# Performance work log

Hardware: AMD Instinct MI355X
Metric: run time of the kernel (lower is better)

The kernel has to match this reference:

```python
import jax, jax.numpy as jnp
import numpy as np

V = 10000   # vocab_size
L = 12      # n_layer
H = 12      # n_head
C = 768     # n_embd
TE = 64     # t_embd
WTE = C - TE
BS = 1024   # block_size
B, T = 4, 1024
D = C // H
EPS = 1e-5


def setup_inputs() -> dict:
    key = jax.random.key(0)
    ks = jax.random.split(key, 12)
    s = 0.02
    def n(k, shape, extra=1.0):
        return jax.random.normal(k, shape, jnp.float32) * (s * extra)
    resid_scale = 1.0 / np.sqrt(2 * L)  # c_proj init std scaling from _init_weights loop
    return {
        'idx': jax.random.randint(ks[0], (B, T), 0, V),
        'ts': jax.random.uniform(ks[1], (B, T), jnp.float32) * 100.0,
        'wte': n(ks[2], (V, WTE)),
        'basis_freq': jnp.asarray(1.0 / 10 ** np.linspace(0, 9, TE), jnp.float32),
        'phase': jnp.zeros((TE,), jnp.float32),
        'wpe': n(ks[3], (BS, C)),
        'ln1_w': jnp.ones((L, C), jnp.float32), 'ln1_b': jnp.zeros((L, C), jnp.float32),
        'qkv_w': n(ks[4], (L, 3 * C, C)), 'qkv_b': jnp.zeros((L, 3 * C), jnp.float32),
        'proj_w': n(ks[5], (L, C, C), resid_scale), 'proj_b': jnp.zeros((L, C), jnp.float32),
        'ln2_w': jnp.ones((L, C), jnp.float32), 'ln2_b': jnp.zeros((L, C), jnp.float32),
        'fc_w': n(ks[6], (L, 4 * C, C)), 'fc_b': jnp.zeros((L, 4 * C), jnp.float32),
        'fc2_w': n(ks[7], (L, C, 4 * C), resid_scale), 'fc2_b': jnp.zeros((L, C), jnp.float32),
        'lnf_w': jnp.ones((C,), jnp.float32), 'lnf_b': jnp.zeros((C,), jnp.float32),
        'lm_w': n(ks[8], (V, C)),
        'tp_w': n(ks[9], (1, C)),
    }


def _ln(x, w, b):
    mu = jnp.mean(x, -1, keepdims=True)
    var = jnp.mean((x - mu) ** 2, -1, keepdims=True)
    return (x - mu) * jax.lax.rsqrt(var + EPS) * w + b


def reference(idx, ts, wte, basis_freq, phase, wpe, ln1_w, ln1_b, qkv_w, qkv_b,
              proj_w, proj_b, ln2_w, ln2_b, fc_w, fc_b, fc2_w, fc2_b,
              lnf_w, lnf_b, lm_w, tp_w):
    Bv, Tv = idx.shape
    tok = wte[idx]                                      # [B,T,C-TE]
    tim = jnp.cos(ts[..., None] * basis_freq + phase)   # TimeEncode -> [B,T,TE]
    x = jnp.concatenate([tok, tim], axis=-1) + wpe[:Tv]
    mask = jnp.tril(jnp.ones((Tv, Tv), bool))
    scale = 1.0 / np.sqrt(D)

    def block(x, p):
        l1w, l1b, qw, qb, pw, pb, l2w, l2b, fw, fb, f2w, f2b = p
        h = _ln(x, l1w, l1b)
        qkv = h @ qw.T + qb                              # [B,T,3C]
        q, k, v = jnp.split(qkv, 3, axis=-1)
        def heads(z):
            return z.reshape(Bv, Tv, H, D).transpose(0, 2, 1, 3)  # [B,H,T,D]
        q, k, v = heads(q), heads(k), heads(v)
        att = jnp.einsum('bhtd,bhsd->bhts', q, k) * scale
        att = jnp.where(mask, att, -jnp.inf)             # causal masked_fill
        att = jax.nn.softmax(att, axis=-1)
        y = jnp.einsum('bhts,bhsd->bhtd', att, v)
        y = y.transpose(0, 2, 1, 3).reshape(Bv, Tv, C)
        x = x + (y @ pw.T + pb)
        h2 = _ln(x, l2w, l2b)
        m = jax.nn.gelu(h2 @ fw.T + fb, approximate=False)  # torch nn.GELU default is exact
        x = x + (m @ f2w.T + f2b)
        return x, None

    x, _ = jax.lax.scan(block, x, (ln1_w, ln1_b, qkv_w, qkv_b, proj_w, proj_b,
                                   ln2_w, ln2_b, fc_w, fc_b, fc2_w, fc2_b))
    x = _ln(x, lnf_w, lnf_b)
    logits = x @ lm_w.T          # [B,T,V]
    tpred = x @ tp_w.T           # [B,T,1]
    return logits, tpred
```

## Files before the change

kernel.cpp:

```cpp
#include <hip/hip_runtime.h>
#include <hip/hip_bf16.h>
#include <math.h>

#define Bb   4
#define Tt   1024
#define Cc   768
#define Hh   12
#define Dd   64
#define Ll   12
#define Vv   10000
#define WTEe 704
#define MTOT 4096

#define QSCALE 0.18033688f

typedef __bf16 bf16x8 __attribute__((ext_vector_type(8)));
typedef float  f32x4  __attribute__((ext_vector_type(4)));
typedef unsigned short u16;

typedef const __attribute__((address_space(1))) void* gptr_t;
typedef __attribute__((address_space(3))) void* lptr_t;

__device__ inline void gload16(const void* g, void* l) {
    __builtin_amdgcn_global_load_lds((gptr_t)g, (lptr_t)l, 16, 0, 0);
}

__device__ inline u16 f2bf(float f) {
    unsigned int u = __float_as_uint(f);
    return (u16)((u + 0x7fffu + ((u >> 16) & 1u)) >> 16);
}
__device__ inline float bf2f(u16 u) { return __uint_as_float(((unsigned)u) << 16); }

__device__ inline float gelu_f(float v) {
    float t = v * (0.797884561f + 0.0356774081f * v * v);
    float e = __expf(2.f * t);
    float th = 1.f - 2.f / (e + 1.f);
    return 0.5f * v * (1.f + th);
}

#if __has_builtin(__builtin_amdgcn_exp2f)
__device__ inline float fast_exp2(float x) { return __builtin_amdgcn_exp2f(x); }
#else
__device__ inline float fast_exp2(float x) { return exp2f(x); }
#endif

#define WAITVM(N)  asm volatile("s_waitcnt vmcnt(" #N ")" ::: "memory")
#define WAITLGKM0() asm volatile("s_waitcnt lgkmcnt(0)" ::: "memory")
#define SCHEDB()   __builtin_amdgcn_sched_barrier(0)
#define SBAR()     __builtin_amdgcn_s_barrier()

__global__ __launch_bounds__(256)
void convert_pack(const float* __restrict__ in, u16* __restrict__ out,
                  int nk8, int K, int rowmod, int scaleLim)
{
    int i = blockIdx.x * 256 + threadIdx.x;
    if (i >= nk8) return;
    int row = (i << 3) / K;
    int col = (i << 3) % K;
    float s = 1.f;
    if (rowmod && (row % rowmod) < scaleLim) s = QSCALE;
    float4 v0 = ((const float4*)in)[2 * i];
    float4 v1 = ((const float4*)in)[2 * i + 1];
    uint4 o;
    o.x = (unsigned)f2bf(v0.x * s) | ((unsigned)f2bf(v0.y * s) << 16);
    o.y = (unsigned)f2bf(v0.z * s) | ((unsigned)f2bf(v0.w * s) << 16);
    o.z = (unsigned)f2bf(v1.x * s) | ((unsigned)f2bf(v1.y * s) << 16);
    o.w = (unsigned)f2bf(v1.z * s) | ((unsigned)f2bf(v1.w * s) << 16);
    int tile = row >> 4, kt = col >> 5;
    int l = (row & 15) | (((col >> 3) & 3) << 4);
    size_t off = (((size_t)tile * (K >> 5) + kt) << 9) + l * 8;
    *(uint4*)(out + off) = o;
}

__global__ __launch_bounds__(256)
void scale_qkvb(const float* __restrict__ in, float* __restrict__ out, int n)
{
    int i = blockIdx.x * 256 + threadIdx.x;
    if (i >= n) return;
    int col = i % (3 * Cc);
    out[i] = in[i] * (col < Cc ? QSCALE : 1.f);
}

__global__ __launch_bounds__(256)
void embed_kernel(const int* __restrict__ idx, const float* __restrict__ ts,
                  const float* __restrict__ wte, const float* __restrict__ freq,
                  const float* __restrict__ ph, const float* __restrict__ wpe,
                  float* __restrict__ x)
{
    const int bt  = blockIdx.x;
    const int t   = bt & (Tt - 1);
    const int tok = idx[bt];
    const float tv = ts[bt];
#pragma unroll
    for (int j = 0; j < 3; ++j) {
        int c = threadIdx.x + (j << 8);
        float val;
        if (c < WTEe) val = wte[(size_t)tok * WTEe + c];
        else {
            int e = c - WTEe;
            val = cosf(tv * freq[e] + ph[e]);
        }
        x[(size_t)bt * Cc + c] = val + wpe[(size_t)t * Cc + c];
    }
}

__global__ __launch_bounds__(256)
void ln_kernel(const float* __restrict__ x, const float* __restrict__ wt,
               const float* __restrict__ bs, u16* __restrict__ out)
{
    const int row = blockIdx.x;
    const int tid = threadIdx.x;
    const float* xr = x + (size_t)row * Cc;
    float v0 = xr[tid], v1 = xr[tid + 256], v2 = xr[tid + 512];
    float s = v0 + v1 + v2;
#pragma unroll
    for (int m = 32; m; m >>= 1) s += __shfl_xor(s, m);
    __shared__ float red[4];
    const int wv = tid >> 6;
    if ((tid & 63) == 0) red[wv] = s;
    __syncthreads();
    float mu = (red[0] + red[1] + red[2] + red[3]) * (1.f / 768.f);
    float d0 = v0 - mu, d1 = v1 - mu, d2 = v2 - mu;
    float s2 = d0 * d0 + d1 * d1 + d2 * d2;
#pragma unroll
    for (int m = 32; m; m >>= 1) s2 += __shfl_xor(s2, m);
    __syncthreads();
    if ((tid & 63) == 0) red[wv] = s2;
    __syncthreads();
    float var = (red[0] + red[1] + red[2] + red[3]) * (1.f / 768.f);
    float rs = rsqrtf(var + 1e-5f);
    u16* orow = out + (size_t)row * Cc;
    orow[tid]       = f2bf(d0 * rs * wt[tid]       + bs[tid]);
    orow[tid + 256] = f2bf(d1 * rs * wt[tid + 256] + bs[tid + 256]);
    orow[tid + 512] = f2bf(d2 * rs * wt[tid + 512] + bs[tid + 512]);
}

__device__ inline void st_out(float* p, size_t o, float v) { p[o] = v; }
__device__ inline void st_out(u16*   p, size_t o, float v) { p[o] = f2bf(v); }

template<int EPI, typename OutT>
__global__ __launch_bounds__(256)
void gemm_bf16(const u16* __restrict__ A, const u16* __restrict__ Wp,
               const float* __restrict__ bias, const float* __restrict__ resid,
               OutT* __restrict__ out, u16* __restrict__ vt, int N, int K)
{
    __shared__ uint4 AF[3][8][64];
    __shared__ uint4 BF[3][8][64];
    const int tid  = threadIdx.x;
    const int lane = tid & 63;
    const int w    = tid >> 6;
    const int wr   = w >> 1, wc = w & 1;
    const int lq   = lane & 15, g = lane >> 4;
    const int m0   = blockIdx.x * 128, n0 = blockIdx.y * 128;
    const int KB   = K >> 5;

    const int arow0 = m0 + (2 * w) * 16 + lq;
    const int arow1 = arow0 + 16;
    const u16* ap0 = A + (size_t)arow0 * K + g * 8;
    const u16* ap1 = A + (size_t)arow1 * K + g * 8;

    int tn0 = (n0 >> 4) + 2 * w, tn1 = tn0 + 1;
    const int tmax = (N >> 4) - 1;
    tn0 = tn0 < tmax ? tn0 : tmax;
    tn1 = tn1 < tmax ? tn1 : tmax;
    const u16* bq0 = Wp + (((size_t)tn0 * KB) << 9) + lane * 8;
    const u16* bq1 = Wp + (((size_t)tn1 * KB) << 9) + lane * 8;

    f32x4 acc[4][4] = {};
    const int nk = KB;

#define GSTAGE(s, sl) do { int kk_ = (s) << 5;                      \
        gload16(ap0 + kk_, &AF[sl][2 * w][lane]);                   \
        gload16(ap1 + kk_, &AF[sl][2 * w + 1][lane]);               \
        gload16(bq0 + ((size_t)(s) << 9), &BF[sl][2 * w][lane]);    \
        gload16(bq1 + ((size_t)(s) << 9), &BF[sl][2 * w + 1][lane]); } while (0)

    GSTAGE(0, 0);
    GSTAGE(1, 1);
    WAITVM(4);
    SCHEDB();
    SBAR();
    SCHEDB();

    int sl = 0;
    for (int t = 0; t < nk; ++t) {
        int sl2 = sl + 2; if (sl2 >= 3) sl2 -= 3;
        if (t + 2 < nk) GSTAGE(t + 2, sl2);

        bf16x8 af[4], bfr[4];
#pragma unroll
        for (int mi = 0; mi < 4; ++mi)
            af[mi] = __builtin_bit_cast(bf16x8, AF[sl][wr * 4 + mi][lane]);
#pragma unroll
        for (int ni = 0; ni < 4; ++ni)
            bfr[ni] = __builtin_bit_cast(bf16x8, BF[sl][wc * 4 + ni][lane]);
        __builtin_amdgcn_s_setprio(1);
#pragma unroll
        for (int mi = 0; mi < 4; ++mi)
#pragma unroll
            for (int ni = 0; ni < 4; ++ni)
                acc[mi][ni] = __builtin_amdgcn_mfma_f32_16x16x32_bf16(
                    af[mi], bfr[ni], acc[mi][ni], 0, 0, 0);
        __builtin_amdgcn_s_setprio(0);

        if (t + 2 < nk) { WAITVM(4); }
        else           { WAITVM(0); }
        SCHEDB();
        SBAR();
        SCHEDB();
        sl = (sl + 1 == 3) ? 0 : sl + 1;
    }
#undef GSTAGE

    if (EPI == 3 && n0 >= 1536) {
#pragma unroll
        for (int mi = 0; mi < 4; ++mi)
#pragma unroll
            for (int ni = 0; ni < 4; ++ni) {
                int col = n0 + wc * 64 + ni * 16 + lq;
                int c2  = col - 1536;
                int hh  = c2 >> 6, dd = c2 & 63;
                int row = m0 + wr * 64 + mi * 16 + g * 4;
                int bb  = row >> 10, tr = row & 1023;
                float bv = bias[col];
                ushort4 o;
                o.x = f2bf(acc[mi][ni][0] + bv);
                o.y = f2bf(acc[mi][ni][1] + bv);
                o.z = f2bf(acc[mi][ni][2] + bv);
                o.w = f2bf(acc[mi][ni][3] + bv);
                *(ushort4*)&vt[(((size_t)bb * Hh + hh) * Dd + dd) * Tt + tr] = o;
            }
        return;
    }

#pragma unroll
    for (int mi = 0; mi < 4; ++mi)
#pragma unroll
        for (int ni = 0; ni < 4; ++ni) {
            int col = n0 + wc * 64 + ni * 16 + lq;
            if (col >= N) continue;
            int row = m0 + wr * 64 + mi * 16 + g * 4;
            float bv = bias ? bias[col] : 0.f;
#pragma unroll
            for (int q = 0; q < 4; ++q) {
                float v = acc[mi][ni][q] + bv;
                size_t o = (size_t)(row + q) * N + col;
                if (EPI == 1) v += resid[o];
                if (EPI == 2) v = gelu_f(v);
                st_out(out, o, v);
            }
        }
}

template<int EPI, typename OutT>
__global__ __launch_bounds__(256)
void gemm_n64(const u16* __restrict__ A, const u16* __restrict__ Wp,
              const float* __restrict__ bias, const float* __restrict__ resid,
              OutT* __restrict__ out, int N, int K)
{
    __shared__ uint4 AF[3][4][64];
    __shared__ uint4 BF[3][8][64];
    const int tid  = threadIdx.x;
    const int lane = tid & 63;
    const int w    = tid >> 6;
    const int wr   = w & 1, wc = w >> 1;
    const int lq   = lane & 15, g = lane >> 4;
    const int m0   = blockIdx.x * 64, n0 = blockIdx.y * 128;
    const int KB   = K >> 5;

    const u16* ap  = A + (size_t)(m0 + w * 16 + lq) * K + g * 8;
    int tn0 = (n0 >> 4) + 2 * w, tn1 = tn0 + 1;
    const int tmax = (N >> 4) - 1;
    tn0 = tn0 < tmax ? tn0 : tmax;
    tn1 = tn1 < tmax ? tn1 : tmax;
    const u16* bq0 = Wp + (((size_t)tn0 * KB) << 9) + lane * 8;
    const u16* bq1 = Wp + (((size_t)tn1 * KB) << 9) + lane * 8;

    f32x4 acc[2][4] = {};
    const int nk = KB;

#define GSTAGE(s, sl) do { int kk_ = (s) << 5;                      \
        gload16(ap  + kk_, &AF[sl][w][lane]);                       \
        gload16(bq0 + ((size_t)(s) << 9), &BF[sl][2 * w][lane]);    \
        gload16(bq1 + ((size_t)(s) << 9), &BF[sl][2 * w + 1][lane]); } while (0)

    GSTAGE(0, 0);
    GSTAGE(1, 1);
    WAITVM(3);
    SCHEDB();
    SBAR();
    SCHEDB();

    int sl = 0;
    for (int t = 0; t < nk; ++t) {
        int sl2 = sl + 2; if (sl2 >= 3) sl2 -= 3;
        if (t + 2 < nk) GSTAGE(t + 2, sl2);

        bf16x8 af[2], bfr[4];
#pragma unroll
        for (int mi = 0; mi < 2; ++mi)
            af[mi] = __builtin_bit_cast(bf16x8, AF[sl][wr * 2 + mi][lane]);
#pragma unroll
        for (int ni = 0; ni < 4; ++ni)
            bfr[ni] = __builtin_bit_cast(bf16x8, BF[sl][wc * 4 + ni][lane]);
        __builtin_amdgcn_s_setprio(1);
#pragma unroll
        for (int mi = 0; mi < 2; ++mi)
#pragma unroll
            for (int ni = 0; ni < 4; ++ni)
                acc[mi][ni] = __builtin_amdgcn_mfma_f32_16x16x32_bf16(
                    af[mi], bfr[ni], acc[mi][ni], 0, 0, 0);
        __builtin_amdgcn_s_setprio(0);

        if (t + 2 < nk) { WAITVM(3); }
        else           { WAITVM(0); }
        SCHEDB();
        SBAR();
        SCHEDB();
        sl = (sl + 1 == 3) ? 0 : sl + 1;
    }
#undef GSTAGE

#pragma unroll
    for (int mi = 0; mi < 2; ++mi)
#pragma unroll
        for (int ni = 0; ni < 4; ++ni) {
            int col = n0 + wc * 64 + ni * 16 + lq;
            if (col >= N) continue;
            int row = m0 + wr * 32 + mi * 16 + g * 4;
            float bv = bias ? bias[col] : 0.f;
#pragma unroll
            for (int q = 0; q < 4; ++q) {
                float v = acc[mi][ni][q] + bv;
                size_t o = (size_t)(row + q) * N + col;
                if (EPI == 1) v += resid[o];
                if (EPI == 2) v = gelu_f(v);
                st_out(out, o, v);
            }
        }
}

template<int EPI, typename OutT>
__global__ __launch_bounds__(512, 2)
void gemm8p(const u16* __restrict__ A, const u16* __restrict__ Wp,
            const float* __restrict__ bias, const float* __restrict__ resid,
            OutT* __restrict__ out, int N, int K)
{
    __shared__ uint4 AF[2][16][2][64];
    __shared__ uint4 BF[2][16][2][64];
    const int tid  = threadIdx.x;
    const int lane = tid & 63;
    const int w    = tid >> 6;
    const int wr   = w >> 2, wc = w & 3;
    const int lq   = lane & 15, g = lane >> 4;
    const int m0   = blockIdx.x * 256, n0 = blockIdx.y * 256;
    const int KB   = K >> 5;

    const int ar0 = m0 + (2 * w) * 16 + lq;
    const u16* aS0 = A + (size_t)ar0 * K + g * 8;
    const u16* aS1 = aS0 + (size_t)16 * K;

    int tn0 = (n0 >> 4) + 2 * w, tn1 = tn0 + 1;
    const int tmax = (N >> 4) - 1;
    tn0 = tn0 < tmax ? tn0 : tmax;
    tn1 = tn1 < tmax ? tn1 : tmax;
    const u16* bq0 = Wp + (((size_t)tn0 * KB) << 9) + lane * 8;
    const u16* bq1 = Wp + (((size_t)tn1 * KB) << 9) + lane * 8;

    f32x4 acc[8][4] = {};
    const int nt = K >> 6;

    gload16(aS0,      &AF[0][2 * w][0][lane]);
    gload16(aS1,      &AF[0][2 * w + 1][0][lane]);
    gload16(bq0,                 &BF[0][2 * w][0][lane]);
    gload16(bq1,                 &BF[0][2 * w + 1][0][lane]);
    gload16(aS0 + 32, &AF[0][2 * w][1][lane]);
    gload16(aS1 + 32, &AF[0][2 * w + 1][1][lane]);
    gload16(bq0 + 512,           &BF[0][2 * w][1][lane]);
    gload16(bq1 + 512,           &BF[0][2 * w + 1][1][lane]);
    WAITVM(0);
    SCHEDB();
    SBAR();

    int buf = 0;
    for (int t = 0; t < nt; ++t) {
        const bool more = (t + 1 < nt);
        const int kn = (t + 1) << 6;
        const size_t bb0 = (size_t)(2 * (t + 1)) << 9;
        bf16x8 a0[4], a1[4], b0[4];

#pragma unroll
        for (int i = 0; i < 4; ++i)
            a0[i] = __builtin_bit_cast(bf16x8, AF[buf][wr * 8 + i][0][lane]);
#pragma unroll
        for (int i = 0; i < 4; ++i)
            b0[i] = __builtin_bit_cast(bf16x8, BF[buf][wc * 4 + i][0][lane]);
        if (more) {
            gload16(aS0 + kn, &AF[buf ^ 1][2 * w][0][lane]);
            gload16(aS1 + kn, &AF[buf ^ 1][2 * w + 1][0][lane]);
        }
        SCHEDB();
        SBAR();
        WAITLGKM0();
        SCHEDB();
        __builtin_amdgcn_s_setprio(1);
#pragma unroll
        for (int mi = 0; mi < 4; ++mi)
#pragma unroll
            for (int ni = 0; ni < 4; ++ni)
                acc[mi][ni] = __builtin_amdgcn_mfma_f32_16x16x32_bf16(
                    a0[mi], b0[ni], acc[mi][ni], 0, 0, 0);
        __builtin_amdgcn_s_setprio(0);
        SBAR();

#pragma unroll
        for (int i = 0; i < 4; ++i)
            a1[i] = __builtin_bit_cast(bf16x8, AF[buf][wr * 8 + 4 + i][0][lane]);
        if (more) {
            gload16(bq0 + bb0, &BF[buf ^ 1][2 * w][0][lane]);
            gload16(bq1 + bb0, &BF[buf ^ 1][2 * w + 1][0][lane]);
        }
        SCHEDB();
        SBAR();
        WAITLGKM0();
        SCHEDB();
        __builtin_amdgcn_s_setprio(1);
#pragma unroll
        for (int mi = 0; mi < 4; ++mi)
#pragma unroll
            for (int ni = 0; ni < 4; ++ni)
                acc[4 + mi][ni] = __builtin_amdgcn_mfma_f32_16x16x32_bf16(
                    a1[mi], b0[ni], acc[4 + mi][ni], 0, 0, 0);
        __builtin_amdgcn_s_setprio(0);
        if (more) { WAITVM(4); } else { WAITVM(0); }
        SCHEDB();
        SBAR();

#pragma unroll
        for (int i = 0; i < 4; ++i)
            a0[i] = __builtin_bit_cast(bf16x8, AF[buf][wr * 8 + i][1][lane]);
#pragma unroll
        for (int i = 0; i < 4; ++i)
            b0[i] = __builtin_bit_cast(bf16x8, BF[buf][wc * 4 + i][1][lane]);
        if (more) {
            gload16(aS0 + kn + 32, &AF[buf ^ 1][2 * w][1][lane]);
            gload16(aS1 + kn + 32, &AF[buf ^ 1][2 * w + 1][1][lane]);
        }
        SCHEDB();
        SBAR();
        WAITLGKM0();
        SCHEDB();
        __builtin_amdgcn_s_setprio(1);
#pragma unroll
        for (int mi = 0; mi < 4; ++mi)
#pragma unroll
            for (int ni = 0; ni < 4; ++ni)
                acc[mi][ni] = __builtin_amdgcn_mfma_f32_16x16x32_bf16(
                    a0[mi], b0[ni], acc[mi][ni], 0, 0, 0);
        __builtin_amdgcn_s_setprio(0);
        SBAR();

#pragma unroll
        for (int i = 0; i < 4; ++i)
            a1[i] = __builtin_bit_cast(bf16x8, AF[buf][wr * 8 + 4 + i][1][lane]);
        if (more) {
            gload16(bq0 + bb0 + 512, &BF[buf ^ 1][2 * w][1][lane]);
            gload16(bq1 + bb0 + 512, &BF[buf ^ 1][2 * w + 1][1][lane]);
        }
        SCHEDB();
        SBAR();
        WAITLGKM0();
        SCHEDB();
        __builtin_amdgcn_s_setprio(1);
#pragma unroll
        for (int mi = 0; mi < 4; ++mi)
#pragma unroll
            for (int ni = 0; ni < 4; ++ni)
                acc[4 + mi][ni] = __builtin_amdgcn_mfma_f32_16x16x32_bf16(
                    a1[mi], b0[ni], acc[4 + mi][ni], 0, 0, 0);
        __builtin_amdgcn_s_setprio(0);
        if (more) { WAITVM(4); } else { WAITVM(0); }
        SCHEDB();
        SBAR();

        buf ^= 1;
    }

#pragma unroll
    for (int mi = 0; mi < 8; ++mi)
#pragma unroll
        for (int ni = 0; ni < 4; ++ni) {
            int col = n0 + wc * 64 + ni * 16 + lq;
            if (col >= N) continue;
            int row = m0 + wr * 128 + mi * 16 + g * 4;
            float bv = bias ? bias[col] : 0.f;
#pragma unroll
            for (int q = 0; q < 4; ++q) {
                float v = acc[mi][ni][q] + bv;
                size_t o = (size_t)(row + q) * N + col;
                if (EPI == 1) v += resid[o];
                if (EPI == 2) v = gelu_f(v);
                st_out(out, o, v);
            }
        }
}

__global__ __launch_bounds__(512)
void attn_mfma(const u16* __restrict__ qkv, const u16* __restrict__ vt,
               u16* __restrict__ y)
{
    __shared__ uint4 KF[2][4][2][64];
    __shared__ uint4 VF[2][4][2][64];

    const int tid  = threadIdx.x;
    const int lane = tid & 63;
    const int w    = tid >> 6;
    const int lq   = lane & 15, g = lane >> 4;
    const int m    = gridDim.x - 1 - blockIdx.x;
    const int bh   = blockIdx.y;
    const int b    = bh / Hh, h = bh % Hh;
    const int wq0  = m * 128 + w * 16;
    const size_t base = (size_t)b * Tt * (3 * Cc);

    const u16* qrow = qkv + base + (size_t)(wq0 + lq) * (3 * Cc) + h * Dd;
    bf16x8 qf0 = __builtin_bit_cast(bf16x8, *(const uint4*)(qrow + g * 8));
    bf16x8 qf1 = __builtin_bit_cast(bf16x8, *(const uint4*)(qrow + 32 + g * 8));

    f32x4 yac[4] = {};
    float lrun = 0.f;

    const int wm = w & 3;
    const u16* kbase = qkv + base + Cc + h * Dd + (size_t)(wm * 16 + lq) * (3 * Cc) + g * 8;
    const u16* vbase = vt + ((size_t)bh * Dd + wm * 16 + lq) * Tt + g * 8;

#define STAGE(c, bi)  do {                                              \
        if (w < 4) {                                                    \
            const u16* kp = kbase + (size_t)(c) * 64 * (3 * Cc);        \
            gload16(kp,      &KF[bi][wm][0][lane]);                     \
            gload16(kp + 32, &KF[bi][wm][1][lane]);                     \
        } else {                                                        \
            const u16* vp = vbase + (c) * 64;                           \
            gload16(vp,      &VF[bi][wm][0][lane]);                     \
            gload16(vp + 32, &VF[bi][wm][1][lane]);                     \
        }                                                               \
    } while (0)

    const int nch = 2 * m + 2;
    STAGE(0, 0);
    WAITVM(0);
    SCHEDB();
    SBAR();

    const int srcb = lq + ((g & 1) << 5);

    int buf = 0;
    for (int c = 0; c < nch; ++c) {
        if (c + 1 < nch) STAGE(c + 1, buf ^ 1);

        f32x4 sc[4] = {};
        __builtin_amdgcn_s_setprio(1);
#pragma unroll
        for (int nt = 0; nt < 4; ++nt) {
            bf16x8 k0 = __builtin_bit_cast(bf16x8, KF[buf][nt][0][lane]);
            bf16x8 k1 = __builtin_bit_cast(bf16x8, KF[buf][nt][1][lane]);
            sc[nt] = __builtin_amdgcn_mfma_f32_16x16x32_bf16(k0, qf0, sc[nt], 0, 0, 0);
            sc[nt] = __builtin_amdgcn_mfma_f32_16x16x32_bf16(k1, qf1, sc[nt], 0, 0, 0);
        }
        __builtin_amdgcn_s_setprio(0);

        const int s0 = c * 64;
        if (s0 + 63 > wq0) {
            const int qg = wq0 + lq;
#pragma unroll
            for (int nt = 0; nt < 4; ++nt) {
                const int kb = s0 + nt * 16 + (g << 2);
#pragma unroll
                for (int j = 0; j < 4; ++j)
                    if (kb + j > qg) sc[nt][j] = -1e30f;
            }
        }

        float ls = 0.f;
#pragma unroll
        for (int nt = 0; nt < 4; ++nt)
#pragma unroll
            for (int j = 0; j < 4; ++j) {
                float p = fast_exp2(sc[nt][j]);
                sc[nt][j] = p;
                ls += p;
            }
        ls += __shfl_xor(ls, 16);
        ls += __shfl_xor(ls, 32);
        lrun += ls;

        unsigned pk[4][2];
#pragma unroll
        for (int nt = 0; nt < 4; ++nt) {
            unsigned u0 = __float_as_uint(sc[nt][0]);
            unsigned u1 = __float_as_uint(sc[nt][1]);
            unsigned u2 = __float_as_uint(sc[nt][2]);
            unsigned u3 = __float_as_uint(sc[nt][3]);
            pk[nt][0] = (u0 >> 16) | (u1 & 0xffff0000u);
            pk[nt][1] = (u2 >> 16) | (u3 & 0xffff0000u);
        }

        unsigned pa0[4], pa1[4];
#pragma unroll
        for (int m2 = 0; m2 < 4; ++m2) {
            int hsel = m2 & 1;
            int src  = srcb + ((m2 >> 1) << 4);
            unsigned lo0 = __shfl(pk[0][hsel], src);
            unsigned hi0 = __shfl(pk[1][hsel], src);
            unsigned lo1 = __shfl(pk[2][hsel], src);
            unsigned hi1 = __shfl(pk[3][hsel], src);
            pa0[m2] = (g >> 1) ? hi0 : lo0;
            pa1[m2] = (g >> 1) ? hi1 : lo1;
        }
        uint4 A0 = make_uint4(pa0[0], pa0[1], pa0[2], pa0[3]);
        uint4 A1 = make_uint4(pa1[0], pa1[1], pa1[2], pa1[3]);
        bf16x8 pA0 = __builtin_bit_cast(bf16x8, A0);
        bf16x8 pA1 = __builtin_bit_cast(bf16x8, A1);

        __builtin_amdgcn_s_setprio(1);
#pragma unroll
        for (int dt = 0; dt < 4; ++dt) {
            bf16x8 vb0 = __builtin_bit_cast(bf16x8, VF[buf][dt][0][lane]);
            bf16x8 vb1 = __builtin_bit_cast(bf16x8, VF[buf][dt][1][lane]);
            yac[dt] = __builtin_amdgcn_mfma_f32_16x16x32_bf16(pA0, vb0, yac[dt], 0, 0, 0);
            yac[dt] = __builtin_amdgcn_mfma_f32_16x16x32_bf16(pA1, vb1, yac[dt], 0, 0, 0);
        }
        __builtin_amdgcn_s_setprio(0);

        if (c + 1 < nch) { WAITVM(0); }
        SCHEDB();
        SBAR();
        buf ^= 1;
    }
#undef STAGE

    f32x4 rl;
#pragma unroll
    for (int j = 0; j < 4; ++j)
        rl[j] = 1.0f / __shfl(lrun, (g << 2) + j);
#pragma unroll
    for (int dt = 0; dt < 4; ++dt)
#pragma unroll
        for (int j = 0; j < 4; ++j)
            y[(size_t)(b * Tt + wq0 + (g << 2) + j) * Cc + h * Dd + dt * 16 + lq]
                = f2bf(yac[dt][j] * rl[j]);
}

__global__ __launch_bounds__(256)
void tpred_kernel(const u16* __restrict__ h, const float* __restrict__ tp,
                  float* __restrict__ out)
{
    const int row  = blockIdx.x * 4 + (threadIdx.x >> 6);
    const int lane = threadIdx.x & 63;
    const u16* hr = h + (size_t)row * Cc;
    float s = 0.f;
#pragma unroll
    for (int j = 0; j < 12; ++j) s += bf2f(hr[lane + (j << 6)]) * tp[lane + (j << 6)];
#pragma unroll
    for (int m = 32; m; m >>= 1) s += __shfl_xor(s, m);
    if (lane == 0) out[row] = s;
}

extern "C" void kernel_launch(void* const* d_in, const int* in_sizes, int n_in,
                              void* d_out, int out_size, void* d_ws, size_t ws_size,
                              hipStream_t stream)
{
    const int*   idx  = (const int*)d_in[0];
    const float* ts   = (const float*)d_in[1];
    const float* wte  = (const float*)d_in[2];
    const float* freq = (const float*)d_in[3];
    const float* ph   = (const float*)d_in[4];
    const float* wpe  = (const float*)d_in[5];
    const float* ln1w = (const float*)d_in[6];
    const float* ln1b = (const float*)d_in[7];
    const float* qkvw = (const float*)d_in[8];
    const float* qkvb = (const float*)d_in[9];
    const float* pw   = (const float*)d_in[10];
    const float* pb   = (const float*)d_in[11];
    const float* ln2w = (const float*)d_in[12];
    const float* ln2b = (const float*)d_in[13];
    const float* fcw  = (const float*)d_in[14];
    const float* fcb  = (const float*)d_in[15];
    const float* f2w  = (const float*)d_in[16];
    const float* f2b  = (const float*)d_in[17];
    const float* lnfw = (const float*)d_in[18];
    const float* lnfb = (const float*)d_in[19];
    const float* lmw  = (const float*)d_in[20];
    const float* tpw  = (const float*)d_in[21];
    float* out = (float*)d_out;

    const int n_qkvw = 3 * Cc * Cc, n_pw = Cc * Cc, n_fcw = 4 * Cc * Cc;

    char* p = (char*)d_ws;
    float* x    = (float*)p;               p += (size_t)MTOT * Cc * 4;
    u16*   qkvB = (u16*)p;                 p += (size_t)MTOT * 3 * Cc * 2;
    u16*   VtB  = (u16*)p;                 p += (size_t)Bb * Hh * Dd * Tt * 2;
    u16*   hB   = (u16*)p;                 p += (size_t)MTOT * Cc * 2;
    u16*   yB   = (u16*)p;                 p += (size_t)MTOT * Cc * 2;
    u16*   mbB  = (u16*)p;                 p += (size_t)MTOT * 4 * Cc * 2;
    u16*   lmwB = (u16*)p;                 p += (size_t)Vv * Cc * 2;
    float* sbias= (float*)p;               p += (size_t)Ll * 3 * Cc * 4;
    char* wbase = p;

    size_t need_big = (size_t)(wbase - (char*)d_ws)
                    + ((size_t)Ll * (n_qkvw + n_pw + 2 * n_fcw)) * 2;
    bool big = ws_size >= need_big;

    u16 *wqA, *wpA, *wfA, *wf2A;
    if (big) {
        wqA  = (u16*)wbase;                wbase += (size_t)Ll * n_qkvw * 2;
        wpA  = (u16*)wbase;                wbase += (size_t)Ll * n_pw * 2;
        wfA  = (u16*)wbase;                wbase += (size_t)Ll * n_fcw * 2;
        wf2A = (u16*)wbase;
    } else {
        wqA  = (u16*)wbase;                wbase += (size_t)n_qkvw * 2;
        wpA  = (u16*)wbase;                wbase += (size_t)n_pw * 2;
        wfA  = (u16*)wbase;                wbase += (size_t)n_fcw * 2;
        wf2A = (u16*)wbase;
    }

    auto pack = [&](const float* src, u16* dst, size_t rows, int K,
                    int rowmod, int scaleLim) {
        int nk8 = (int)(rows * K / 8);
        convert_pack<<<(nk8 + 255) / 256, 256, 0, stream>>>(
            src, dst, nk8, K, rowmod, scaleLim);
    };

    pack(lmw, lmwB, Vv, Cc, 0, 0);
    {
        int nb = Ll * 3 * Cc;
        scale_qkvb<<<(nb + 255) / 256, 256, 0, stream>>>(qkvb, sbias, nb);
    }
    if (big) {
        pack(qkvw, wqA,  (size_t)Ll * 3 * Cc, Cc, 3 * Cc, Cc);
        pack(pw,   wpA,  (size_t)Ll * Cc,     Cc, 0, 0);
        pack(fcw,  wfA,  (size_t)Ll * 4 * Cc, Cc, 0, 0);
        pack(f2w,  wf2A, (size_t)Ll * Cc, 4 * Cc, 0, 0);
    }
    embed_kernel<<<MTOT, 256, 0, stream>>>(idx, ts, wte, freq, ph, wpe, x);

    for (int l = 0; l < Ll; ++l) {
        u16 *wqB, *wpB, *wfB, *wf2B;
        if (big) {
            wqB  = wqA  + (size_t)l * n_qkvw;
            wpB  = wpA  + (size_t)l * n_pw;
            wfB  = wfA  + (size_t)l * n_fcw;
            wf2B = wf2A + (size_t)l * n_fcw;
        } else {
            wqB = wqA; wpB = wpA; wfB = wfA; wf2B = wf2A;
            pack(qkvw + (size_t)l * n_qkvw, wqB, 3 * Cc, Cc, 3 * Cc, Cc);
            pack(pw   + (size_t)l * n_pw,   wpB, Cc,     Cc, 0, 0);
            pack(fcw  + (size_t)l * n_fcw,  wfB, 4 * Cc, Cc, 0, 0);
            pack(f2w  + (size_t)l * n_fcw,  wf2B, Cc, 4 * Cc, 0, 0);
        }

        ln_kernel<<<MTOT, 256, 0, stream>>>(x, ln1w + l * Cc, ln1b + l * Cc, hB);
        gemm_bf16<3, u16><<<dim3(32, 18), 256, 0, stream>>>(
            hB, wqB, sbias + (size_t)l * 3 * Cc, nullptr, qkvB, VtB, 3 * Cc, Cc);
        attn_mfma<<<dim3(Tt / 128, Bb * Hh), 512, 0, stream>>>(qkvB, VtB, yB);
        gemm_n64<1, float><<<dim3(64, 6), 256, 0, stream>>>(
            yB, wpB, pb + (size_t)l * Cc, x, x, Cc, Cc);
        ln_kernel<<<MTOT, 256, 0, stream>>>(x, ln2w + l * Cc, ln2b + l * Cc, hB);
        gemm_bf16<2, u16><<<dim3(32, 24), 256, 0, stream>>>(
            hB, wfB, fcb + (size_t)l * 4 * Cc, nullptr, mbB, nullptr, 4 * Cc, Cc);
        gemm_n64<1, float><<<dim3(64, 6), 256, 0, stream>>>(
            mbB, wf2B, f2b + (size_t)l * Cc, x, x, Cc, 4 * Cc);
    }

    ln_kernel<<<MTOT, 256, 0, stream>>>(x, lnfw, lnfb, hB);
    gemm8p<0, float><<<dim3(16, 40), 512, 0, stream>>>(
        hB, lmwB, nullptr, nullptr, out, Vv, Cc);
    tpred_kernel<<<MTOT / 4, 256, 0, stream>>>(hB, tpw, out + (size_t)MTOT * Vv);
}
```

Measured before the change: 2.764 ms.

## Emit LayerNorm output in MFMA-fragment-packed layout for GEMM A operands

Adds a LayerNorm kernel that handles 16 rows per block and writes bf16 output directly in the 16x32 fragment-tiled layout the GEMMs consume. The QKV, FC and LM-head GEMMs then load A tiles as contiguous 1KB chunks instead of strided row reads, and tpred indexes the packed layout. This aims to make A-operand global loads fully contiguous and to cut LN launch count. The single-pass variance (E[x^2]-mu^2) slightly changes numerics.

```diff
diff --git a/kernel.cpp b/kernel.cpp
--- a/kernel.cpp
+++ b/kernel.cpp
@@ -135,10 +135,69 @@
     orow[tid + 512] = f2bf(d2 * rs * wt[tid + 512] + bs[tid + 512]);
 }
 
+__global__ __launch_bounds__(256)
+void ln_pack16(const float* __restrict__ x, const float* __restrict__ wt,
+               const float* __restrict__ bs, u16* __restrict__ out)
+{
+    __shared__ float mus[16], rss[16];
+    const int tid  = threadIdx.x;
+    const int lane = tid & 63;
+    const int w    = tid >> 6;
+    const int tile = blockIdx.x;
+    const int r0   = tile << 4;
+
+#pragma unroll
+    for (int rr = 0; rr < 4; ++rr) {
+        const int row = r0 + w * 4 + rr;
+        const float* xr = x + (size_t)row * Cc;
+        float s = 0.f, s2 = 0.f;
+#pragma unroll
+        for (int j = 0; j < 12; ++j) {
+            float v = xr[lane + (j << 6)];
+            s += v; s2 += v * v;
+        }
+#pragma unroll
+        for (int m = 32; m; m >>= 1) {
+            s  += __shfl_xor(s, m);
+            s2 += __shfl_xor(s2, m);
+        }
+        if (lane == 0) {
+            float mu = s * (1.f / 768.f);
+            float var = s2 * (1.f / 768.f) - mu * mu;
+            mus[w * 4 + rr] = mu;
+            rss[w * 4 + rr] = rsqrtf(var + 1e-5f);
+        }
+    }
+    __syncthreads();
+
+    u16* ob = out + ((size_t)tile * 24 << 9);
+#pragma unroll
+    for (int it = 0; it < 6; ++it) {
+        int c   = tid + (it << 8);
+        int kt  = c >> 6, l = c & 63;
+        int row = l & 15, g = l >> 4;
+        int col = kt * 32 + g * 8;
+        float mu = mus[row], rs = rss[row];
+        const float* xp = x + (size_t)(r0 + row) * Cc + col;
+        float4 a = *(const float4*)xp;
+        float4 bq = *(const float4*)(xp + 4);
+        ushort o[8];
+        o[0] = f2bf((a.x - mu) * rs * wt[col]     + bs[col]);
+        o[1] = f2bf((a.y - mu) * rs * wt[col + 1] + bs[col + 1]);
+        o[2] = f2bf((a.z - mu) * rs * wt[col + 2] + bs[col + 2]);
+        o[3] = f2bf((a.w - mu) * rs * wt[col + 3] + bs[col + 3]);
+        o[4] = f2bf((bq.x - mu) * rs * wt[col + 4] + bs[col + 4]);
+        o[5] = f2bf((bq.y - mu) * rs * wt[col + 5] + bs[col + 5]);
+        o[6] = f2bf((bq.z - mu) * rs * wt[col + 6] + bs[col + 6]);
+        o[7] = f2bf((bq.w - mu) * rs * wt[col + 7] + bs[col + 7]);
+        *(uint4*)(ob + ((size_t)kt << 9) + l * 8) = *(uint4*)o;
+    }
+}
+
 __device__ inline void st_out(float* p, size_t o, float v) { p[o] = v; }
 __device__ inline void st_out(u16*   p, size_t o, float v) { p[o] = f2bf(v); }
 
-template<int EPI, typename OutT>
+template<int EPI, int APK, typename OutT>
 __global__ __launch_bounds__(256)
 void gemm_bf16(const u16* __restrict__ A, const u16* __restrict__ Wp,
                const float* __restrict__ bias, const float* __restrict__ resid,
@@ -154,10 +213,14 @@
     const int m0   = blockIdx.x * 128, n0 = blockIdx.y * 128;
     const int KB   = K >> 5;
 
-    const int arow0 = m0 + (2 * w) * 16 + lq;
-    const int arow1 = arow0 + 16;
-    const u16* ap0 = A + (size_t)arow0 * K + g * 8;
-    const u16* ap1 = A + (size_t)arow1 * K + g * 8;
+    const u16 *ap0, *ap1;
+    if (APK) {
+        ap0 = A + ((((size_t)(m0 >> 4) + 2 * w) * KB) << 9) + lane * 8;
+        ap1 = ap0 + ((size_t)KB << 9);
+    } else {
+        ap0 = A + (size_t)(m0 + (2 * w) * 16 + lq) * K + g * 8;
+        ap1 = ap0 + (size_t)16 * K;
+    }
 
     int tn0 = (n0 >> 4) + 2 * w, tn1 = tn0 + 1;
     const int tmax = (N >> 4) - 1;
@@ -169,10 +232,15 @@
     f32x4 acc[4][4] = {};
     const int nk = KB;
 
-#define GSTAGE(s, sl) do { int kk_ = (s) << 5;                      \
-        gload16(ap0 + kk_, &AF[sl][2 * w][lane]);                   \
-        gload16(ap1 + kk_, &AF[sl][2 * w + 1][lane]);               \
-        gload16(bq0 + ((size_t)(s) << 9), &BF[sl][2 * w][lane]);    \
+#define GSTAGE(s, sl) do {                                               \
+        if (APK) {                                                       \
+            gload16(ap0 + ((size_t)(s) << 9), &AF[sl][2 * w][lane]);     \
+            gload16(ap1 + ((size_t)(s) << 9), &AF[sl][2 * w + 1][lane]); \
+        } else {                                                         \
+            gload16(ap0 + ((s) << 5), &AF[sl][2 * w][lane]);             \
+            gload16(ap1 + ((s) << 5), &AF[sl][2 * w + 1][lane]);         \
+        }                                                                \
+        gload16(bq0 + ((size_t)(s) << 9), &BF[sl][2 * w][lane]);         \
         gload16(bq1 + ((size_t)(s) << 9), &BF[sl][2 * w + 1][lane]); } while (0)
 
     GSTAGE(0, 0);
@@ -342,7 +410,7 @@
 
 template<int EPI, typename OutT>
 __global__ __launch_bounds__(512, 2)
-void gemm8p(const u16* __restrict__ A, const u16* __restrict__ Wp,
+void gemm8p(const u16* __restrict__ Apk, const u16* __restrict__ Wp,
             const float* __restrict__ bias, const float* __restrict__ resid,
             OutT* __restrict__ out, int N, int K)
 {
@@ -356,9 +424,8 @@
     const int m0   = blockIdx.x * 256, n0 = blockIdx.y * 256;
     const int KB   = K >> 5;
 
-    const int ar0 = m0 + (2 * w) * 16 + lq;
-    const u16* aS0 = A + (size_t)ar0 * K + g * 8;
-    const u16* aS1 = aS0 + (size_t)16 * K;
+    const u16* aq0 = Apk + ((((size_t)(m0 >> 4) + 2 * w) * KB) << 9) + lane * 8;
+    const u16* aq1 = aq0 + ((size_t)KB << 9);
 
     int tn0 = (n0 >> 4) + 2 * w, tn1 = tn0 + 1;
     const int tmax = (N >> 4) - 1;
@@ -370,14 +437,14 @@
     f32x4 acc[8][4] = {};
     const int nt = K >> 6;
 
-    gload16(aS0,      &AF[0][2 * w][0][lane]);
-    gload16(aS1,      &AF[0][2 * w + 1][0][lane]);
-    gload16(bq0,                 &BF[0][2 * w][0][lane]);
-    gload16(bq1,                 &BF[0][2 * w + 1][0][lane]);
-    gload16(aS0 + 32, &AF[0][2 * w][1][lane]);
-    gload16(aS1 + 32, &AF[0][2 * w + 1][1][lane]);
-    gload16(bq0 + 512,           &BF[0][2 * w][1][lane]);
-    gload16(bq1 + 512,           &BF[0][2 * w + 1][1][lane]);
+    gload16(aq0,       &AF[0][2 * w][0][lane]);
+    gload16(aq1,       &AF[0][2 * w + 1][0][lane]);
+    gload16(bq0,       &BF[0][2 * w][0][lane]);
+    gload16(bq1,       &BF[0][2 * w + 1][0][lane]);
+    gload16(aq0 + 512, &AF[0][2 * w][1][lane]);
+    gload16(aq1 + 512, &AF[0][2 * w + 1][1][lane]);
+    gload16(bq0 + 512, &BF[0][2 * w][1][lane]);
+    gload16(bq1 + 512, &BF[0][2 * w + 1][1][lane]);
     WAITVM(0);
     SCHEDB();
     SBAR();
@@ -385,7 +452,6 @@
     int buf = 0;
     for (int t = 0; t < nt; ++t) {
         const bool more = (t + 1 < nt);
-        const int kn = (t + 1) << 6;
         const size_t bb0 = (size_t)(2 * (t + 1)) << 9;
         bf16x8 a0[4], a1[4], b0[4];
 
@@ -396,8 +462,8 @@
         for (int i = 0; i < 4; ++i)
             b0[i] = __builtin_bit_cast(bf16x8, BF[buf][wc * 4 + i][0][lane]);
         if (more) {
-            gload16(aS0 + kn, &AF[buf ^ 1][2 * w][0][lane]);
-            gload16(aS1 + kn, &AF[buf ^ 1][2 * w + 1][0][lane]);
+            gload16(aq0 + bb0, &AF[buf ^ 1][2 * w][0][lane]);
+            gload16(aq1 + bb0, &AF[buf ^ 1][2 * w + 1][0][lane]);
         }
         SCHEDB();
         SBAR();
@@ -443,8 +509,8 @@
         for (int i = 0; i < 4; ++i)
             b0[i] = __builtin_bit_cast(bf16x8, BF[buf][wc * 4 + i][1][lane]);
         if (more) {
-            gload16(aS0 + kn + 32, &AF[buf ^ 1][2 * w][1][lane]);
-            gload16(aS1 + kn + 32, &AF[buf ^ 1][2 * w + 1][1][lane]);
+            gload16(aq0 + bb0 + 512, &AF[buf ^ 1][2 * w][1][lane]);
+            gload16(aq1 + bb0 + 512, &AF[buf ^ 1][2 * w + 1][1][lane]);
         }
         SCHEDB();
         SBAR();
@@ -651,15 +717,20 @@
 }
 
 __global__ __launch_bounds__(256)
-void tpred_kernel(const u16* __restrict__ h, const float* __restrict__ tp,
+void tpred_kernel(const u16* __restrict__ hp, const float* __restrict__ tp,
                   float* __restrict__ out)
 {
     const int row  = blockIdx.x * 4 + (threadIdx.x >> 6);
     const int lane = threadIdx.x & 63;
-    const u16* hr = h + (size_t)row * Cc;
+    const int tile = row >> 4, r15 = row & 15;
+    const u16* tb = hp + ((size_t)tile * 24 << 9);
     float s = 0.f;
 #pragma unroll
-    for (int j = 0; j < 12; ++j) s += bf2f(hr[lane + (j << 6)]) * tp[lane + (j << 6)];
+    for (int j = 0; j < 12; ++j) {
+        int col = lane + (j << 6);
+        int kt = col >> 5, g = (col >> 3) & 3, e = col & 7;
+        s += bf2f(tb[((size_t)kt << 9) + (r15 | (g << 4)) * 8 + e]) * tp[col];
+    }
 #pragma unroll
     for (int m = 32; m; m >>= 1) s += __shfl_xor(s, m);
     if (lane == 0) out[row] = s;
@@ -758,20 +829,20 @@
             pack(f2w  + (size_t)l * n_fcw,  wf2B, Cc, 4 * Cc, 0, 0);
         }
 
-        ln_kernel<<<MTOT, 256, 0, stream>>>(x, ln1w + l * Cc, ln1b + l * Cc, hB);
-        gemm_bf16<3, u16><<<dim3(32, 18), 256, 0, stream>>>(
+        ln_pack16<<<MTOT / 16, 256, 0, stream>>>(x, ln1w + l * Cc, ln1b + l * Cc, hB);
+        gemm_bf16<3, 1, u16><<<dim3(32, 18), 256, 0, stream>>>(
             hB, wqB, sbias + (size_t)l * 3 * Cc, nullptr, qkvB, VtB, 3 * Cc, Cc);
         attn_mfma<<<dim3(Tt / 128, Bb * Hh), 512, 0, stream>>>(qkvB, VtB, yB);
         gemm_n64<1, float><<<dim3(64, 6), 256, 0, stream>>>(
             yB, wpB, pb + (size_t)l * Cc, x, x, Cc, Cc);
-        ln_kernel<<<MTOT, 256, 0, stream>>>(x, ln2w + l * Cc, ln2b + l * Cc, hB);
-        gemm_bf16<2, u16><<<dim3(32, 24), 256, 0, stream>>>(
+        ln_pack16<<<MTOT / 16, 256, 0, stream>>>(x, ln2w + l * Cc, ln2b + l * Cc, hB);
+        gemm_bf16<2, 1, u16><<<dim3(32, 24), 256, 0, stream>>>(
             hB, wfB, fcb + (size_t)l * 4 * Cc, nullptr, mbB, nullptr, 4 * Cc, Cc);
         gemm_n64<1, float><<<dim3(64, 6), 256, 0, stream>>>(
             mbB, wf2B, f2b + (size_t)l * Cc, x, x, Cc, 4 * Cc);
     }
 
-    ln_kernel<<<MTOT, 256, 0, stream>>>(x, lnfw, lnfb, hB);
+    ln_pack16<<<MTOT / 16, 256, 0, stream>>>(x, lnfw, lnfb, hB);
     gemm8p<0, float><<<dim3(16, 40), 512, 0, stream>>>(
         hB, lmwB, nullptr, nullptr, out, Vv, Cc);
     tpred_kernel<<<MTOT / 4, 256, 0, stream>>>(hB, tpw, out + (size_t)MTOT * Vv);
```

Result: faster. 2.698 ms (-2.4%).
